# Kernel tuning notes

Measured on AMD Instinct MI355X. Metric: run time of the kernel, lower is better.

The kernel has to match this reference:

```python
import math
import jax, jax.numpy as jnp
import numpy as np

B, L, Q, H = 4, 256, 128, 1024
TYPES = 32
LABELS = TYPES + 1
FACTOR = math.sqrt(H)


def _init(key, shape, fan_in):
    return jax.random.normal(key, shape, jnp.float32) / math.sqrt(fan_in)


def _gelu(x):
    # torch nn.GELU default = exact erf form
    return jax.nn.gelu(x, approximate=False)


def setup_inputs() -> dict:
    key = jax.random.key(0)
    ks = jax.random.split(key, 12)
    lengths = jax.random.randint(ks[0], (B,), L // 2, L + 1)
    batch_masks = jnp.arange(L)[None, :] < lengths[:, None]  # [B,L] bool
    return {
        "batch_hiddens": jax.random.normal(ks[1], (B, L, H), jnp.float32),
        "batch_masks": batch_masks,
        "queries": jax.random.normal(ks[2], (B, Q, H), jnp.float32),
        "queries_locs": jax.random.uniform(ks[3], (B, Q, 2), jnp.float32) * L,
        "queries_logits": jax.random.normal(ks[4], (B, Q, LABELS), jnp.float32),
        "cls_w1": _init(ks[5], (H, H // 2), H),
        "cls_b1": jnp.zeros((H // 2,), jnp.float32),
        "cls_w2": _init(ks[6], (H // 2, LABELS), H // 2),
        "cls_b2": jnp.zeros((LABELS,), jnp.float32),
        "tq_w": _init(ks[7], (H, 2 * H), H),
        "tq_b": jnp.zeros((2 * H,), jnp.float32),
        "tc_w": _init(ks[8], (H, 2 * H), H),
        "tc_b": jnp.zeros((2 * H,), jnp.float32),
        "loc_w1": _init(ks[9], (H, H // 2), H),
        "loc_b1": jnp.zeros((H // 2,), jnp.float32),
        "loc_w2": _init(ks[10], (H // 2, 6), H // 2) * 0.1,
        "loc_b2": jnp.zeros((6,), jnp.float32),
    }


def reference(batch_hiddens, batch_masks, queries, queries_locs, queries_logits,
              cls_w1, cls_b1, cls_w2, cls_b2, tq_w, tq_b, tc_w, tc_b,
              loc_w1, loc_b1, loc_w2, loc_b2):
    # Classifier: label probabilities fused with prior logits
    cls_logits = _gelu(queries @ cls_w1 + cls_b1) @ cls_w2 + cls_b2  # [B,Q,LABELS]
    labels_pros = jax.nn.softmax(queries_logits + cls_logits, axis=-1)

    # Bilinear start/end channel scores
    qh = (queries @ tq_w + tq_b).reshape(B, Q, 2, H)        # [B,Q,2,H]
    ch = (batch_hiddens @ tc_w + tc_b).reshape(B, L, 2, H)  # [B,L,2,H]
    score = jnp.einsum('bqch,bvch->bcqv', qh, ch) / FACTOR  # [B,2,Q,L]
    score = jnp.where(batch_masks[:, None, None, :], score, -1e8)

    # Span-pair table: all (start i <= end j); P = L*(L+1)/2
    i_idx, j_idx = jnp.triu_indices(L)
    score_p = score[:, 0][:, :, i_idx] + score[:, 1][:, :, j_idx]  # [B,Q,P]
    mask_p = batch_masks[:, j_idx]                                  # [B,P]

    # Locator: per-query Gaussian-like quadratic-form span weight
    loc_out = _gelu(queries @ loc_w1 + loc_b1) @ loc_w2 + loc_b2  # [B,Q,6]
    offsets = loc_out[..., :2]
    fac = loc_out[..., 2:].reshape(B, Q, 2, 2)
    fac = fac @ jnp.swapaxes(fac, -1, -2)  # PSD factor matrix [B,Q,2,2]
    centers = queries_locs + offsets        # [B,Q,2]
    pairs_f = jnp.stack([i_idx, j_idx], axis=-1).astype(jnp.float32)  # [P,2]
    delta = pairs_f[None, None] - centers[:, :, None, :]              # [B,Q,P,2]
    quad = jnp.einsum('bqpi,bqij,bqpj->bqp', delta, fac, delta)       # >= 0
    weight = jnp.exp(-quad) * mask_p[:, None, :].astype(score_p.dtype)

    # Weighted (fused) softmax over span pairs
    m = jnp.max(score_p, axis=-1, keepdims=True)
    e = weight * jnp.exp(score_p - m)
    locs_pros = e / (jnp.sum(e, axis=-1, keepdims=True) + 1e-12)
    return labels_pros, locs_pros
```

## Files before the change

kernel.cpp:

```cpp
#include <hip/hip_runtime.h>
#include <math.h>

typedef _Float16 f16;
typedef __attribute__((ext_vector_type(4))) _Float16 f16x4;
typedef __attribute__((ext_vector_type(8))) _Float16 f16x8;
typedef __attribute__((ext_vector_type(4))) float f32x4;

#define Bn 4
#define Ln 256
#define Qn 128
#define Hn 1024
#define LBL 33
#define POUT 32896

__device__ __forceinline__ float gelu_exact(float x){
    return 0.5f * x * (1.0f + erff(x * 0.70710678118654752f));
}

__device__ __forceinline__ bool mask_at(const void* m, int idx, unsigned u0){
    if (u0 == 0x01010101u) return ((const unsigned char*)m)[idx] != 0;
    if (u0 == 0x3f800000u) return ((const float*)m)[idx] != 0.0f;
    return ((const int*)m)[idx] != 0;
}

__device__ __forceinline__ void gload16(const void* g, void* l){
    __builtin_amdgcn_global_load_lds(
        (const __attribute__((address_space(1))) unsigned int*)g,
        (__attribute__((address_space(3))) unsigned int*)l, 16, 0, 0);
}

__global__ __launch_bounds__(256) void prep(
    const float* __restrict__ q, const float* __restrict__ h,
    const float* __restrict__ cls_w1, const float* __restrict__ loc_w1,
    const float* __restrict__ tq_w,  const float* __restrict__ tc_w,
    f16* __restrict__ qf, f16* __restrict__ hf,
    f16* __restrict__ Wq_t, f16* __restrict__ Wc_t)
{
    const int bx = blockIdx.x, t = threadIdx.x;
    if (bx < 1536) {
        if (bx < 512) {
            const int gid = bx*256 + t;
            const float4 v = ((const float4*)q)[gid];
            f16x4 o; o[0]=(f16)v.x; o[1]=(f16)v.y; o[2]=(f16)v.z; o[3]=(f16)v.w;
            *(f16x4*)&qf[(size_t)gid*4] = o;
        } else {
            const int gid = (bx-512)*256 + t;
            const float4 v = ((const float4*)h)[gid];
            f16x4 o; o[0]=(f16)v.x; o[1]=(f16)v.y; o[2]=(f16)v.z; o[3]=(f16)v.w;
            *(f16x4*)&hf[(size_t)gid*4] = o;
        }
        return;
    }
    const int tile = bx - 1536;
    const float* src; f16* dst; int id, lg;
    if      (tile < 256)  { id = tile;        src = cls_w1; dst = Wq_t;                     lg = 4; }
    else if (tile < 512)  { id = tile - 256;  src = loc_w1; dst = Wq_t + (size_t)512*1024;  lg = 4; }
    else if (tile < 1536) { id = tile - 512;  src = tq_w;   dst = Wq_t + (size_t)1024*1024; lg = 6; }
    else                  { id = tile - 1536; src = tc_w;   dst = Wc_t;                     lg = 6; }
    const int N  = 32 << lg;
    const int n0 = (id & ((1<<lg)-1)) * 32;
    const int k0 = (id >> lg) * 64;

    __shared__ float X[64][33];
    const int rr = t >> 3, c4 = (t & 7) * 4;
    const float4 v0 = *(const float4*)&src[(size_t)(k0 + rr)      * N + n0 + c4];
    const float4 v1 = *(const float4*)&src[(size_t)(k0 + rr + 32) * N + n0 + c4];
    X[rr   ][c4+0] = v0.x; X[rr   ][c4+1] = v0.y; X[rr   ][c4+2] = v0.z; X[rr   ][c4+3] = v0.w;
    X[rr+32][c4+0] = v1.x; X[rr+32][c4+1] = v1.y; X[rr+32][c4+2] = v1.z; X[rr+32][c4+3] = v1.w;
    __syncthreads();
    const int n = t >> 3, kc = (t & 7) * 8;
    f16x8 o;
    #pragma unroll
    for (int u = 0; u < 8; u++) o[u] = (f16)X[kc + u][n];
    *(f16x8*)&dst[(size_t)(n0 + n) * 1024 + k0 + kc] = o;
}

__global__ __launch_bounds__(256) void gemm128(
    const f16* __restrict__ Aq, const f16* __restrict__ Ac,
    const f16* __restrict__ Wq, const f16* __restrict__ Wc,
    const float* __restrict__ cb1, const float* __restrict__ lb1,
    const float* __restrict__ tqb, const float* __restrict__ tcb,
    float* __restrict__ X1, float* __restrict__ X2,
    f16* __restrict__ qh, f16* __restrict__ chh)
{
    __shared__ __align__(16) f16 Ah[128*64];
    __shared__ __align__(16) f16 Bh[128*64];
    const int tid = threadIdx.x;
    const int w = tid >> 6, lane = tid & 63;
    const int wr = w >> 1, wcc = w & 1;
    const int lr = lane & 15, hi = lane >> 4;

    const int bx = blockIdx.x;
    const f16 *A, *Bt;
    int bm, bn, qside;
    if (bx < 96) { qside = 1; bm = bx / 24; bn = bx % 24; A = Aq; Bt = Wq; }
    else         { qside = 0; const int ix = bx - 96; bm = ix >> 4; bn = ix & 15; A = Ac; Bt = Wc; }

    const int lr8   = lane >> 3;
    const int lslot = (lane & 7) ^ lr8;
    const f16* Ag = A  + (size_t)(bm*128 + w*32) * 1024;
    const f16* Bg = Bt + (size_t)(bn*128 + w*32) * 1024;
    f16* AhW = &Ah[(w*32)*64];
    f16* BhW = &Bh[(w*32)*64];

    f32x4 acc[4][4] = {};

    for (int k0 = 0; k0 < 1024; k0 += 64) {
        #pragma unroll
        for (int i = 0; i < 4; i++) {
            gload16(Ag + (size_t)(i*8 + lr8)*1024 + k0 + lslot*8, AhW + i*8*64);
            gload16(Bg + (size_t)(i*8 + lr8)*1024 + k0 + lslot*8, BhW + i*8*64);
        }
        __syncthreads();
        #pragma unroll
        for (int ks = 0; ks < 2; ks++) {
            f16x8 a[4], b[4];
            #pragma unroll
            for (int mf = 0; mf < 4; mf++) {
                const int row = wr*64 + mf*16 + lr;
                const int sl  = (ks*4 + hi) ^ (lr & 7);
                a[mf] = *(const f16x8*)&Ah[row*64 + sl*8];
            }
            #pragma unroll
            for (int nf = 0; nf < 4; nf++) {
                const int row = wcc*64 + nf*16 + lr;
                const int sl  = (ks*4 + hi) ^ (lr & 7);
                b[nf] = *(const f16x8*)&Bh[row*64 + sl*8];
            }
            #pragma unroll
            for (int mf = 0; mf < 4; mf++)
                #pragma unroll
                for (int nf = 0; nf < 4; nf++)
                    acc[mf][nf] = __builtin_amdgcn_mfma_f32_16x16x32_f16(a[mf], b[nf], acc[mf][nf], 0, 0, 0);
        }
        __syncthreads();
    }

    const int r0 = hi * 4;
    #pragma unroll
    for (int nf = 0; nf < 4; nf++) {
        const int colg = bn*128 + wcc*64 + nf*16 + lr;
        if (qside) {
            if (bn < 4) {
                const float bv = cb1[colg];
                #pragma unroll
                for (int mf = 0; mf < 4; mf++)
                    #pragma unroll
                    for (int r = 0; r < 4; r++) {
                        const int row = bm*128 + wr*64 + mf*16 + r0 + r;
                        X1[(size_t)row*512 + colg] = gelu_exact(acc[mf][nf][r] + bv);
                    }
            } else if (bn < 8) {
                const int c2 = colg - 512;
                const float bv = lb1[c2];
                #pragma unroll
                for (int mf = 0; mf < 4; mf++)
                    #pragma unroll
                    for (int r = 0; r < 4; r++) {
                        const int row = bm*128 + wr*64 + mf*16 + r0 + r;
                        X2[(size_t)row*512 + c2] = gelu_exact(acc[mf][nf][r] + bv);
                    }
            } else {
                const int c2 = colg - 1024;
                const float bv = tqb[c2];
                #pragma unroll
                for (int mf = 0; mf < 4; mf++)
                    #pragma unroll
                    for (int r = 0; r < 4; r++) {
                        const int row = bm*128 + wr*64 + mf*16 + r0 + r;
                        qh[(size_t)row*2048 + c2] = (f16)(acc[mf][nf][r] + bv);
                    }
            }
        } else {
            const float bv = tcb[colg];
            #pragma unroll
            for (int mf = 0; mf < 4; mf++)
                #pragma unroll
                for (int r = 0; r < 4; r++) {
                    const int row = bm*128 + wr*64 + mf*16 + r0 + r;
                    chh[(size_t)row*2048 + colg] = (f16)(acc[mf][nf][r] + bv);
                }
        }
    }
}

__global__ __launch_bounds__(256) void score_heads(
    const f16* __restrict__ qh, const f16* __restrict__ chh,
    const void* __restrict__ maskp, float* __restrict__ score,
    const float* __restrict__ X1, const float* __restrict__ cls_w2,
    const float* __restrict__ cls_b2, const float* __restrict__ qlog, float* __restrict__ out0,
    const float* __restrict__ X2, const float* __restrict__ loc_w2,
    const float* __restrict__ loc_b2, const float* __restrict__ qlocs, float* __restrict__ geo)
{
    __shared__ __align__(16) char smem[64*72*2*2 + 64];
    const int bx = blockIdx.x, tid = threadIdx.x;

    if (bx < 64) {
        f16* Ah = (f16*)smem;
        f16* Bh = Ah + 64*72;
        const int bc = bx & 7, b = bc >> 1, c = bc & 1;
        const int n0 = ((bx >> 3) & 3) * 64;
        const int m0 = (bx >> 5) * 64;
        const f16* Aq = qh  + (size_t)b*Qn*2048 + c*1024;
        const f16* Bv = chh + (size_t)b*Ln*2048 + c*1024;

        const int w = tid >> 6, lane = tid & 63;
        const int wr = w >> 1, wc = w & 1;
        const int lr = lane & 15, lk = (lane >> 4) * 8;
        const int rr = tid >> 3, gg = (tid & 7) * 8;

        f32x4 acc[2][2] = {};

        for (int k0 = 0; k0 < 1024; k0 += 64) {
            *(f16x8*)&Ah[(rr   )*72 + gg] = *(const f16x8*)(Aq + (size_t)(m0+rr   )*2048 + k0 + gg);
            *(f16x8*)&Ah[(rr+32)*72 + gg] = *(const f16x8*)(Aq + (size_t)(m0+rr+32)*2048 + k0 + gg);
            *(f16x8*)&Bh[(rr   )*72 + gg] = *(const f16x8*)(Bv + (size_t)(n0+rr   )*2048 + k0 + gg);
            *(f16x8*)&Bh[(rr+32)*72 + gg] = *(const f16x8*)(Bv + (size_t)(n0+rr+32)*2048 + k0 + gg);
            __syncthreads();
            #pragma unroll
            for (int ks=0; ks<64; ks+=32){
                f16x8 a[2], b2[2];
                #pragma unroll
                for (int mf=0; mf<2; mf++) a[mf]  = *(f16x8*)&Ah[(wr*32+mf*16+lr)*72 + ks+lk];
                #pragma unroll
                for (int nf=0; nf<2; nf++) b2[nf] = *(f16x8*)&Bh[(wc*32+nf*16+lr)*72 + ks+lk];
                #pragma unroll
                for (int mf=0; mf<2; mf++)
                    #pragma unroll
                    for (int nf=0; nf<2; nf++)
                        acc[mf][nf] = __builtin_amdgcn_mfma_f32_16x16x32_f16(a[mf], b2[nf], acc[mf][nf], 0, 0, 0);
            }
            __syncthreads();
        }

        const unsigned u0 = *(const unsigned*)maskp;
        const int r0 = (lane >> 4) * 4;
        #pragma unroll
        for (int nf=0; nf<2; nf++){
            const int v = n0 + wc*32 + nf*16 + lr;
            const bool mv = mask_at(maskp, b*Ln + v, u0);
            #pragma unroll
            for (int mf=0; mf<2; mf++){
                #pragma unroll
                for (int r=0; r<4; r++){
                    const int q = m0 + wr*32 + mf*16 + r0 + r;
                    float val = mv ? (acc[mf][nf][r] * 0.03125f) : -100000000.0f;
                    score[((size_t)(b*2+c)*Qn + q)*Ln + v] = val;
                }
            }
        }
    } else if (bx < 576) {
        float* xr = (float*)smem;
        float* lg = xr + 512;
        float* sc = lg + 64;
        const int row = bx - 64, t = tid;
        xr[t]       = X1[(size_t)row*512 + t];
        xr[t + 256] = X1[(size_t)row*512 + t + 256];
        __syncthreads();
        const int c = t >> 2, s = t & 3;
        float acc = 0.0f;
        if (c < LBL){
            for (int k = s*128; k < (s+1)*128; k++) acc += xr[k] * cls_w2[(size_t)k*LBL + c];
        }
        acc += __shfl_down(acc, 1);
        acc += __shfl_down(acc, 2);
        if (s == 0 && c < LBL) lg[c] = acc + cls_b2[c] + qlog[(size_t)row*LBL + c];
        __syncthreads();
        if (t == 0){
            float mx = -1e30f;
            for (int k=0;k<LBL;k++) mx = fmaxf(mx, lg[k]);
            float sm = 0.0f;
            for (int k=0;k<LBL;k++) sm += __expf(lg[k]-mx);
            sc[0] = mx; sc[1] = 1.0f / sm;
        }
        __syncthreads();
        if (t < LBL) out0[(size_t)row*LBL + t] = __expf(lg[t]-sc[0]) * sc[1];
    } else {
        float* xr = (float*)smem;
        float* lg = xr + 512;
        const int row = bx - 576, t = tid;
        xr[t]       = X2[(size_t)row*512 + t];
        xr[t + 256] = X2[(size_t)row*512 + t + 256];
        __syncthreads();
        const int c = t >> 5, s = t & 31;
        float acc = 0.0f;
        if (c < 6){
            for (int k = s*16; k < (s+1)*16; k++) acc += xr[k] * loc_w2[(size_t)k*6 + c];
        }
        #pragma unroll
        for (int off=1; off<32; off<<=1) acc += __shfl_down(acc, off);
        if (s == 0 && c < 6) lg[c] = acc + loc_b2[c];
        __syncthreads();
        if (t == 0){
            const float o0=lg[0], o1=lg[1], f0=lg[2], f1=lg[3], f2=lg[4], f3=lg[5];
            geo[(size_t)row*5+0] = qlocs[(size_t)row*2+0] + o0;
            geo[(size_t)row*5+1] = qlocs[(size_t)row*2+1] + o1;
            geo[(size_t)row*5+2] = f0*f0 + f1*f1;
            geo[(size_t)row*5+3] = f0*f2 + f1*f3;
            geo[(size_t)row*5+4] = f2*f2 + f3*f3;
        }
    }
}

__global__ __launch_bounds__(1024) void pair_fused(
    const float* __restrict__ score, const float* __restrict__ geo,
    float* __restrict__ out1)
{
    const int bq = blockIdx.x, b = bq >> 7, t = threadIdx.x;
    __shared__ float s0[256], s1[256];
    __shared__ float2 RG[256];
    __shared__ float T[256];
    __shared__ float red[16];
    __shared__ float bcv;

    const float* sc0 = score + ((size_t)(b*2)*Qn + (bq & 127))*Ln;
    if (t < 256)      s0[t]       = sc0[t];
    else if (t < 512) s1[t - 256] = sc0[(size_t)Qn*Ln + (t - 256)];
    __syncthreads();

    const int lane = t & 63;
    const float4 s1v = *(const float4*)&s1[lane*4];
    const float4 s0v = *(const float4*)&s0[lane*4];
    float sfx = fmaxf(fmaxf(s1v.x, s1v.y), fmaxf(s1v.z, s1v.w));
    #pragma unroll
    for (int off = 1; off < 64; off <<= 1) {
        const int src = (lane + off < 64) ? (lane + off) : 63;
        const float v = __shfl(sfx, src, 64);
        if (lane + off < 64) sfx = fmaxf(sfx, v);
    }
    float nxt = __shfl(sfx, (lane < 63) ? (lane + 1) : 63, 64);
    if (lane == 63) nxt = -3.0e38f;
    float run = fmaxf(nxt, s1v.w);
    float cand = s0v.w + run;
    run = fmaxf(run, s1v.z); cand = fmaxf(cand, s0v.z + run);
    run = fmaxf(run, s1v.y); cand = fmaxf(cand, s0v.y + run);
    run = fmaxf(run, s1v.x); cand = fmaxf(cand, s0v.x + run);
    #pragma unroll
    for (int off = 1; off < 64; off <<= 1) cand = fmaxf(cand, __shfl_xor(cand, off, 64));
    const float m = cand;

    const float c0  = geo[(size_t)bq*5+0], c1  = geo[(size_t)bq*5+1];
    const float F00 = geo[(size_t)bq*5+2], F01 = geo[(size_t)bq*5+3], F11 = geo[(size_t)bq*5+4];

    if (t < 256) {
        const float d0 = (float)t - c0;
        const float nG = -2.0f * F01 * d0;
        const float Rv = s0[t] - F00 * d0 * d0 - m;
        RG[t] = make_float2(Rv - nG * c1, nG);
        const float d1 = (float)t - c1;
        T[t] = s1[t] - F11 * d1 * d1;
    }
    __syncthreads();

    const int g = t >> 8, l = t & 255;
    const int rp0 = g * 32;

    float lsum = 0.0f;
    float ev[32];
    float ex = 0.0f;

    #pragma unroll
    for (int k = 0; k < 32; k++) {
        const int rp = rp0 + k;
        const bool r2 = (l + rp > 255);
        const int i = r2 ? (255 - rp) : rp;
        const int j = r2 ? (l - 1) : (rp + l);
        const float2 rg = RG[i];
        const float e = __expf(fmaf(rg.y, (float)j, rg.x) + T[j]);
        lsum += e;
        ev[k] = e;
    }
    if (t < 128) {
        const int i = 128 + t;
        const float2 rg = RG[i];
        ex = __expf(fmaf(rg.y, 255.0f, rg.x) + T[255]);
        lsum += ex;
    }

    #pragma unroll
    for (int off = 1; off < 64; off <<= 1) lsum += __shfl_xor(lsum, off, 64);
    if (lane == 0) red[t >> 6] = lsum;
    __syncthreads();
    if (t == 0) {
        float tot = 0.0f;
        #pragma unroll
        for (int k = 0; k < 16; k++) tot += red[k];
        bcv = 1.0f / (tot + 1e-12f);
    }
    __syncthreads();
    const float inv = bcv;

    float* op = out1 + (size_t)bq * POUT;
    #pragma unroll
    for (int k = 0; k < 32; k++) {
        const int rp = rp0 + k;
        const bool r2 = (l + rp > 255);
        const int i2 = 255 - rp;
        const int tri1 = (rp * (513 - rp)) >> 1;
        const int tri2 = ((i2 * (513 - i2)) >> 1) - (256 - rp);
        op[(r2 ? tri2 : tri1) + l] = ev[k] * inv;
    }
    if (t < 128) {
        const int i = 128 + t;
        op[((i * (513 - i)) >> 1) + 127 - t] = ex * inv;
    }
}

extern "C" void kernel_launch(void* const* d_in, const int* in_sizes, int n_in,
                              void* d_out, int out_size, void* d_ws, size_t ws_size,
                              hipStream_t stream)
{
    const float* hiddens = (const float*)d_in[0];
    const void*  masks   = d_in[1];
    const float* queries = (const float*)d_in[2];
    const float* qlocs   = (const float*)d_in[3];
    const float* qlogits = (const float*)d_in[4];
    const float* cls_w1  = (const float*)d_in[5];
    const float* cls_b1  = (const float*)d_in[6];
    const float* cls_w2  = (const float*)d_in[7];
    const float* cls_b2  = (const float*)d_in[8];
    const float* tq_w    = (const float*)d_in[9];
    const float* tq_b    = (const float*)d_in[10];
    const float* tc_w    = (const float*)d_in[11];
    const float* tc_b    = (const float*)d_in[12];
    const float* loc_w1  = (const float*)d_in[13];
    const float* loc_b1  = (const float*)d_in[14];
    const float* loc_w2  = (const float*)d_in[15];
    const float* loc_b2  = (const float*)d_in[16];

    char* ws = (char*)d_ws;
    f16*   qf16  = (f16*)  (ws);
    f16*   hf16  = (f16*)  (ws + (1u<<20));
    float* X1    = (float*)(ws + (3u<<20));
    float* X2    = (float*)(ws + (4u<<20));
    f16*   qh    = (f16*)  (ws + (5u<<20));
    float* score = (float*)(ws + (7u<<20));
    float* geo   = (float*)(ws + (8u<<20));

    float* out0 = (float*)d_out;
    float* out1 = out0 + (size_t)Bn*Qn*LBL;

    f16* Wq_t = (f16*)out1;
    f16* Wc_t = (f16*)((char*)out1 + 6291456);
    f16* chh  = (f16*)((char*)out1 + 6291456 + 4194304);

    prep<<<dim3(4096), 256, 0, stream>>>(queries, hiddens, cls_w1, loc_w1, tq_w, tc_w,
                                         qf16, hf16, Wq_t, Wc_t);
    gemm128<<<dim3(224), 256, 0, stream>>>(qf16, hf16, Wq_t, Wc_t,
                                           cls_b1, loc_b1, tq_b, tc_b,
                                           X1, X2, qh, chh);
    score_heads<<<dim3(1088), 256, 0, stream>>>(qh, chh, masks, score,
                                                X1, cls_w2, cls_b2, qlogits, out0,
                                                X2, loc_w2, loc_b2, qlocs, geo);
    pair_fused<<<dim3(Bn*Qn), 1024, 0, stream>>>(score, geo, out1);
}
```

Before: 78.75 us.

## Double-buffer GEMM shared tiles and split-K the bilinear score GEMM

The main projection GEMM now double-buffers its LDS tiles, issuing async global-to-LDS loads for the next K slice while MFMAs run on the current one. The score GEMM is split four ways along K to give 256 blocks instead of 64, with register-prefetched double-buffered tiles. It writes partial sums that pair_fused later adds up and scales and masks. This is meant to hide load latency and fill more CUs, at the cost of extra LDS, partial-score traffic and a reduction step in the final kernel.

```diff
diff --git a/kernel.cpp b/kernel.cpp
--- a/kernel.cpp
+++ b/kernel.cpp
@@ -12,6 +12,7 @@
 #define Hn 1024
 #define LBL 33
 #define POUT 32896
+#define SPSTRIDE 262144
 
 __device__ __forceinline__ float gelu_exact(float x){
     return 0.5f * x * (1.0f + erff(x * 0.70710678118654752f));
@@ -83,8 +84,8 @@
     float* __restrict__ X1, float* __restrict__ X2,
     f16* __restrict__ qh, f16* __restrict__ chh)
 {
-    __shared__ __align__(16) f16 Ah[128*64];
-    __shared__ __align__(16) f16 Bh[128*64];
+    __shared__ __align__(16) f16 Ah[2][128*64];
+    __shared__ __align__(16) f16 Bh[2][128*64];
     const int tid = threadIdx.x;
     const int w = tid >> 6, lane = tid & 63;
     const int wr = w >> 1, wcc = w & 1;
@@ -100,18 +101,27 @@
     const int lslot = (lane & 7) ^ lr8;
     const f16* Ag = A  + (size_t)(bm*128 + w*32) * 1024;
     const f16* Bg = Bt + (size_t)(bn*128 + w*32) * 1024;
-    f16* AhW = &Ah[(w*32)*64];
-    f16* BhW = &Bh[(w*32)*64];
+    const int wofs = (w*32)*64;
 
     f32x4 acc[4][4] = {};
 
-    for (int k0 = 0; k0 < 1024; k0 += 64) {
-        #pragma unroll
-        for (int i = 0; i < 4; i++) {
-            gload16(Ag + (size_t)(i*8 + lr8)*1024 + k0 + lslot*8, AhW + i*8*64);
-            gload16(Bg + (size_t)(i*8 + lr8)*1024 + k0 + lslot*8, BhW + i*8*64);
-        }
-        __syncthreads();
+    #pragma unroll
+    for (int i = 0; i < 4; i++) {
+        gload16(Ag + (size_t)(i*8 + lr8)*1024 + lslot*8, &Ah[0][wofs + i*8*64]);
+        gload16(Bg + (size_t)(i*8 + lr8)*1024 + lslot*8, &Bh[0][wofs + i*8*64]);
+    }
+    __syncthreads();
+
+    int cur = 0;
+    for (int s = 0; s < 16; ++s) {
+        if (s < 15) {
+            const int k1 = (s + 1) * 64;
+            #pragma unroll
+            for (int i = 0; i < 4; i++) {
+                gload16(Ag + (size_t)(i*8 + lr8)*1024 + k1 + lslot*8, &Ah[cur^1][wofs + i*8*64]);
+                gload16(Bg + (size_t)(i*8 + lr8)*1024 + k1 + lslot*8, &Bh[cur^1][wofs + i*8*64]);
+            }
+        }
         #pragma unroll
         for (int ks = 0; ks < 2; ks++) {
             f16x8 a[4], b[4];
@@ -119,13 +129,13 @@
             for (int mf = 0; mf < 4; mf++) {
                 const int row = wr*64 + mf*16 + lr;
                 const int sl  = (ks*4 + hi) ^ (lr & 7);
-                a[mf] = *(const f16x8*)&Ah[row*64 + sl*8];
+                a[mf] = *(const f16x8*)&Ah[cur][row*64 + sl*8];
             }
             #pragma unroll
             for (int nf = 0; nf < 4; nf++) {
                 const int row = wcc*64 + nf*16 + lr;
                 const int sl  = (ks*4 + hi) ^ (lr & 7);
-                b[nf] = *(const f16x8*)&Bh[row*64 + sl*8];
+                b[nf] = *(const f16x8*)&Bh[cur][row*64 + sl*8];
             }
             #pragma unroll
             for (int mf = 0; mf < 4; mf++)
@@ -134,6 +144,7 @@
                     acc[mf][nf] = __builtin_amdgcn_mfma_f32_16x16x32_f16(a[mf], b[nf], acc[mf][nf], 0, 0, 0);
         }
         __syncthreads();
+        cur ^= 1;
     }
 
     const int r0 = hi * 4;
@@ -186,23 +197,23 @@
 
 __global__ __launch_bounds__(256) void score_heads(
     const f16* __restrict__ qh, const f16* __restrict__ chh,
-    const void* __restrict__ maskp, float* __restrict__ score,
+    float* __restrict__ scorep,
     const float* __restrict__ X1, const float* __restrict__ cls_w2,
     const float* __restrict__ cls_b2, const float* __restrict__ qlog, float* __restrict__ out0,
     const float* __restrict__ X2, const float* __restrict__ loc_w2,
     const float* __restrict__ loc_b2, const float* __restrict__ qlocs, float* __restrict__ geo)
 {
-    __shared__ __align__(16) char smem[64*72*2*2 + 64];
+    __shared__ __align__(16) f16 sAh[2][64*72];
+    __shared__ __align__(16) f16 sBh[2][64*72];
     const int bx = blockIdx.x, tid = threadIdx.x;
 
-    if (bx < 64) {
-        f16* Ah = (f16*)smem;
-        f16* Bh = Ah + 64*72;
-        const int bc = bx & 7, b = bc >> 1, c = bc & 1;
-        const int n0 = ((bx >> 3) & 3) * 64;
-        const int m0 = (bx >> 5) * 64;
-        const f16* Aq = qh  + (size_t)b*Qn*2048 + c*1024;
-        const f16* Bv = chh + (size_t)b*Ln*2048 + c*1024;
+    if (bx < 256) {
+        const int kq = bx >> 6, r = bx & 63;
+        const int bc = r & 7, b = bc >> 1, c = bc & 1;
+        const int n0 = ((r >> 3) & 3) * 64;
+        const int m0 = (r >> 5) * 64;
+        const f16* Aq = qh  + (size_t)b*Qn*2048 + c*1024 + kq*256;
+        const f16* Bv = chh + (size_t)b*Ln*2048 + c*1024 + kq*256;
 
         const int w = tid >> 6, lane = tid & 63;
         const int wr = w >> 1, wc = w & 1;
@@ -211,19 +222,32 @@
 
         f32x4 acc[2][2] = {};
 
-        for (int k0 = 0; k0 < 1024; k0 += 64) {
-            *(f16x8*)&Ah[(rr   )*72 + gg] = *(const f16x8*)(Aq + (size_t)(m0+rr   )*2048 + k0 + gg);
-            *(f16x8*)&Ah[(rr+32)*72 + gg] = *(const f16x8*)(Aq + (size_t)(m0+rr+32)*2048 + k0 + gg);
-            *(f16x8*)&Bh[(rr   )*72 + gg] = *(const f16x8*)(Bv + (size_t)(n0+rr   )*2048 + k0 + gg);
-            *(f16x8*)&Bh[(rr+32)*72 + gg] = *(const f16x8*)(Bv + (size_t)(n0+rr+32)*2048 + k0 + gg);
+        f16x8 ra0 = *(const f16x8*)(Aq + (size_t)(m0+rr   )*2048 + gg);
+        f16x8 ra1 = *(const f16x8*)(Aq + (size_t)(m0+rr+32)*2048 + gg);
+        f16x8 rb0 = *(const f16x8*)(Bv + (size_t)(n0+rr   )*2048 + gg);
+        f16x8 rb1 = *(const f16x8*)(Bv + (size_t)(n0+rr+32)*2048 + gg);
+
+        int cur = 0;
+        for (int s = 0; s < 4; ++s) {
+            *(f16x8*)&sAh[cur][(rr   )*72 + gg] = ra0;
+            *(f16x8*)&sAh[cur][(rr+32)*72 + gg] = ra1;
+            *(f16x8*)&sBh[cur][(rr   )*72 + gg] = rb0;
+            *(f16x8*)&sBh[cur][(rr+32)*72 + gg] = rb1;
+            if (s < 3) {
+                const int k1 = (s + 1) * 64;
+                ra0 = *(const f16x8*)(Aq + (size_t)(m0+rr   )*2048 + k1 + gg);
+                ra1 = *(const f16x8*)(Aq + (size_t)(m0+rr+32)*2048 + k1 + gg);
+                rb0 = *(const f16x8*)(Bv + (size_t)(n0+rr   )*2048 + k1 + gg);
+                rb1 = *(const f16x8*)(Bv + (size_t)(n0+rr+32)*2048 + k1 + gg);
+            }
             __syncthreads();
             #pragma unroll
-            for (int ks=0; ks<64; ks+=32){
+            for (int ks = 0; ks < 64; ks += 32){
                 f16x8 a[2], b2[2];
                 #pragma unroll
-                for (int mf=0; mf<2; mf++) a[mf]  = *(f16x8*)&Ah[(wr*32+mf*16+lr)*72 + ks+lk];
-                #pragma unroll
-                for (int nf=0; nf<2; nf++) b2[nf] = *(f16x8*)&Bh[(wc*32+nf*16+lr)*72 + ks+lk];
+                for (int mf=0; mf<2; mf++) a[mf]  = *(f16x8*)&sAh[cur][(wr*32+mf*16+lr)*72 + ks+lk];
+                #pragma unroll
+                for (int nf=0; nf<2; nf++) b2[nf] = *(f16x8*)&sBh[cur][(wc*32+nf*16+lr)*72 + ks+lk];
                 #pragma unroll
                 for (int mf=0; mf<2; mf++)
                     #pragma unroll
@@ -231,29 +255,28 @@
                         acc[mf][nf] = __builtin_amdgcn_mfma_f32_16x16x32_f16(a[mf], b2[nf], acc[mf][nf], 0, 0, 0);
             }
             __syncthreads();
-        }
-
-        const unsigned u0 = *(const unsigned*)maskp;
+            cur ^= 1;
+        }
+
+        float* op = scorep + (size_t)kq * SPSTRIDE;
         const int r0 = (lane >> 4) * 4;
         #pragma unroll
         for (int nf=0; nf<2; nf++){
             const int v = n0 + wc*32 + nf*16 + lr;
-            const bool mv = mask_at(maskp, b*Ln + v, u0);
             #pragma unroll
             for (int mf=0; mf<2; mf++){
                 #pragma unroll
-                for (int r=0; r<4; r++){
-                    const int q = m0 + wr*32 + mf*16 + r0 + r;
-                    float val = mv ? (acc[mf][nf][r] * 0.03125f) : -100000000.0f;
-                    score[((size_t)(b*2+c)*Qn + q)*Ln + v] = val;
+                for (int rr2=0; rr2<4; rr2++){
+                    const int q = m0 + wr*32 + mf*16 + r0 + rr2;
+                    op[((size_t)(b*2+c)*Qn + q)*Ln + v] = acc[mf][nf][rr2];
                 }
             }
         }
-    } else if (bx < 576) {
-        float* xr = (float*)smem;
+    } else if (bx < 768) {
+        float* xr = (float*)sAh;
         float* lg = xr + 512;
         float* sc = lg + 64;
-        const int row = bx - 64, t = tid;
+        const int row = bx - 256, t = tid;
         xr[t]       = X1[(size_t)row*512 + t];
         xr[t + 256] = X1[(size_t)row*512 + t + 256];
         __syncthreads();
@@ -276,9 +299,9 @@
         __syncthreads();
         if (t < LBL) out0[(size_t)row*LBL + t] = __expf(lg[t]-sc[0]) * sc[1];
     } else {
-        float* xr = (float*)smem;
+        float* xr = (float*)sAh;
         float* lg = xr + 512;
-        const int row = bx - 576, t = tid;
+        const int row = bx - 768, t = tid;
         xr[t]       = X2[(size_t)row*512 + t];
         xr[t + 256] = X2[(size_t)row*512 + t + 256];
         __syncthreads();
@@ -303,8 +326,8 @@
 }
 
 __global__ __launch_bounds__(1024) void pair_fused(
-    const float* __restrict__ score, const float* __restrict__ geo,
-    float* __restrict__ out1)
+    const float* __restrict__ scorep, const void* __restrict__ maskp,
+    const float* __restrict__ geo, float* __restrict__ out1)
 {
     const int bq = blockIdx.x, b = bq >> 7, t = threadIdx.x;
     __shared__ float s0[256], s1[256];
@@ -313,9 +336,17 @@
     __shared__ float red[16];
     __shared__ float bcv;
 
-    const float* sc0 = score + ((size_t)(b*2)*Qn + (bq & 127))*Ln;
-    if (t < 256)      s0[t]       = sc0[t];
-    else if (t < 512) s1[t - 256] = sc0[(size_t)Qn*Ln + (t - 256)];
+    const unsigned u0 = *(const unsigned*)maskp;
+    const float* sp = scorep + ((size_t)(b*2)*Qn + (bq & 127))*Ln;
+    if (t < 512) {
+        const int col = t & 255;
+        const size_t ofs = (t < 256) ? 0 : (size_t)Qn*Ln;
+        const float d = sp[ofs + col] + sp[ofs + col + SPSTRIDE]
+                      + sp[ofs + col + 2*SPSTRIDE] + sp[ofs + col + 3*SPSTRIDE];
+        const bool mv = mask_at(maskp, b*Ln + col, u0);
+        const float v = mv ? d * 0.03125f : -100000000.0f;
+        if (t < 256) s0[col] = v; else s1[col] = v;
+    }
     __syncthreads();
 
     const int lane = t & 63;
@@ -429,13 +460,13 @@
     const float* loc_b2  = (const float*)d_in[16];
 
     char* ws = (char*)d_ws;
-    f16*   qf16  = (f16*)  (ws);
-    f16*   hf16  = (f16*)  (ws + (1u<<20));
-    float* X1    = (float*)(ws + (3u<<20));
-    float* X2    = (float*)(ws + (4u<<20));
-    f16*   qh    = (f16*)  (ws + (5u<<20));
-    float* score = (float*)(ws + (7u<<20));
-    float* geo   = (float*)(ws + (8u<<20));
+    f16*   qf16   = (f16*)  (ws);
+    f16*   hf16   = (f16*)  (ws + (1u<<20));
+    float* X1     = (float*)(ws + (3u<<20));
+    float* X2     = (float*)(ws + (4u<<20));
+    f16*   qh     = (f16*)  (ws + (5u<<20));
+    float* scorep = (float*)(ws + (7u<<20));
+    float* geo    = (float*)(ws + (11u<<20));
 
     float* out0 = (float*)d_out;
     float* out1 = out0 + (size_t)Bn*Qn*LBL;
@@ -449,8 +480,8 @@
     gemm128<<<dim3(224), 256, 0, stream>>>(qf16, hf16, Wq_t, Wc_t,
                                            cls_b1, loc_b1, tq_b, tc_b,
                                            X1, X2, qh, chh);
-    score_heads<<<dim3(1088), 256, 0, stream>>>(qh, chh, masks, score,
+    score_heads<<<dim3(1280), 256, 0, stream>>>(qh, chh, scorep,
                                                 X1, cls_w2, cls_b2, qlogits, out0,
                                                 X2, loc_w2, loc_b2, qlocs, geo);
-    pair_fused<<<dim3(Bn*Qn), 1024, 0, stream>>>(score, geo, out1);
-}
+    pair_fused<<<dim3(Bn*Qn), 1024, 0, stream>>>(scorep, masks, geo, out1);
+}
```

Result: slower. 83.29 us (+5.8%).
